# Kernel optimization log

Measured on AMD Instinct MI355X. Metric: run time of the kernel, lower is better.

## Reference

```python
import jax, jax.numpy as jnp
import numpy as np

B, H, W = 64, 512, 512
CD = 400                      # center_dims
MS_H = MS_W = 10              # max shifts
EPS = 1e-8
C_X = (H - CD) // 2           # 56
C_Y = (W - CD) // 2           # 56


def _conv_valid(x, k):
    # x: [B,h,w,1], k: [kh,kw,1,1] -> VALID conv, stride 1
    return jax.lax.conv_general_dilated(
        x, k, window_strides=(1, 1), padding='VALID',
        dimension_numbers=('NHWC', 'HWIO', 'NHWC'))


def setup_inputs() -> dict:
    key = jax.random.key(0)
    k1, k2 = jax.random.split(key)
    # smooth low-frequency template (so NCC peak neighborhood is positive -> log() finite)
    coarse = jax.random.normal(k1, (32, 32), dtype=jnp.float32)
    template = jax.image.resize(coarse, (H, W), method='bilinear')
    template = template - template.min() + 1.0  # keep positive-ish intensities
    noise = 0.05 * jax.random.normal(k2, (B, H, W, 1), dtype=jnp.float32)
    x = template[None, :, :, None] + noise
    return {'x': x, 'template': template}


def reference(x, template):
    # --- template normalization (init-time in the TF layer) ---
    tmpl = template[MS_W + C_X: H - (MS_W + C_X), MS_H + C_Y: W - (MS_H + C_Y)]  # [380,380]
    tmpl = tmpl[:, :, None, None].astype(jnp.float32)                            # HWIO
    t_zm = tmpl - jnp.mean(tmpl, axis=(0, 1), keepdims=True)
    t_var = jnp.sum(jnp.square(t_zm), axis=(0, 1), keepdims=True) + EPS          # [1,1,1,1]

    # --- image normalization ---
    Xc = x[:, C_X:H - C_X, C_Y:W - C_Y, :]                                       # [B,400,400,1]
    imgs_zm = Xc - jnp.mean(Xc, axis=(1, 2), keepdims=True)
    ones_k = jnp.ones_like(tmpl)
    localsum_sq = _conv_valid(jnp.square(Xc), ones_k)                            # [B,21,21,1]
    localsum = _conv_valid(Xc, ones_k)
    n_t = float(np.prod(tmpl.shape))
    imgs_var = localsum_sq - jnp.square(localsum) / n_t + EPS
    imgs_var = jnp.where(imgs_var < 0, jnp.zeros_like(imgs_var), imgs_var)

    # --- NCC ---
    denominator = jnp.sqrt(t_var * imgs_var)
    numerator = _conv_valid(imgs_zm, t_zm)
    ncc = numerator / denominator
    ncc = jnp.where(jnp.isnan(ncc), jnp.zeros_like(ncc), ncc)                    # [B,21,21,1]

    # --- integer argmax + gaussian (log-parabola) subpixel interpolation ---
    ncc2 = ncc[..., 0]                                                           # [B,21,21]
    ww = ncc2.shape[2]
    am = jnp.argmax(ncc2.reshape(B, -1), axis=1)
    sh_x = (am // ww).astype(jnp.int32)
    sh_y = (am % ww).astype(jnp.int32)
    log_ncc = jnp.log(ncc2)
    bidx = jnp.arange(B)

    def g(dx, dy):
        return log_ncc[bidx, sh_x + dx, sh_y + dy]

    log_xm1_y = g(-1, 0); log_xp1_y = g(1, 0)
    log_x_ym1 = g(0, -1); log_x_yp1 = g(0, 1)
    four_log_xy = 4.0 * g(0, 0)
    sh_x_n = (-(sh_x - MS_H)).astype(jnp.float32) - (log_xm1_y - log_xp1_y) / (
        2.0 * log_xm1_y - four_log_xy + 2.0 * log_xp1_y)
    sh_y_n = (-(sh_y - MS_W)).astype(jnp.float32) - (log_x_ym1 - log_x_yp1) / (
        2.0 * log_x_ym1 - four_log_xy + 2.0 * log_x_yp1)

    # --- bilinear translate: translations=[dx,dy]=[sh_y_n, sh_x_n]; out(r,c)=in(r-dy, c-dx), fill 0 ---
    def warp_one(img, dy, dx):
        rr = jnp.arange(H, dtype=jnp.float32)[:, None] - dy    # [H,1]
        cc = jnp.arange(W, dtype=jnp.float32)[None, :] - dx    # [1,W]
        r0 = jnp.floor(rr); c0 = jnp.floor(cc)
        wr = rr - r0; wc = cc - c0
        r0i = jnp.broadcast_to(r0.astype(jnp.int32), (H, W))
        c0i = jnp.broadcast_to(c0.astype(jnp.int32), (H, W))

        def samp(ri, ci):
            valid = (ri >= 0) & (ri < H) & (ci >= 0) & (ci < W)
            v = img[jnp.clip(ri, 0, H - 1), jnp.clip(ci, 0, W - 1)]
            return jnp.where(valid, v, 0.0)

        v00 = samp(r0i, c0i); v01 = samp(r0i, c0i + 1)
        v10 = samp(r0i + 1, c0i); v11 = samp(r0i + 1, c0i + 1)
        return (v00 * (1 - wr) * (1 - wc) + v01 * (1 - wr) * wc
                + v10 * wr * (1 - wc) + v11 * wr * wc)

    warped = jax.vmap(warp_one)(x[..., 0], sh_x_n, sh_y_n)     # [B,H,W]
    # transpose [0,2,1] then flatten, matching the TF layer's output layout
    return jnp.transpose(warped, (0, 2, 1)).reshape(B, H * W)
```

## Files before the change

### kernel.cpp

```cpp
#include <hip/hip_runtime.h>
#include <math.h>

#define HH 512
#define WW 512
#define NB 64
#define CXY 56
#define TOFF 66
#define TN 380
#define XN 400
#define NL 21
#define N_T 144400.0f
#define EPSF 1e-8f
#define NUT 32
#define SXS 424

#define TPART_S   0
#define TPART_S2  384
#define TSTATS    768
#define ROWSUM    1024
#define ROWSUMSQ  (ROWSUM + 537600)
#define CCPART2   1024
#define LOCALSUM  1076224
#define LOCALSQ   (LOCALSUM + 28224)
#define SHIFTS    1132672
#define SHIFTSI   (SHIFTS + 128)
#define EXACTN    (SHIFTSI + 128)
#define TSHIFT_F  (EXACTN + 384)
#define XF16      (TSHIFT_F + 1677312)

typedef _Float16 half2_t __attribute__((ext_vector_type(2)));
typedef _Float16 f16x8 __attribute__((ext_vector_type(8)));
typedef float f32x4 __attribute__((ext_vector_type(4)));

__global__ __launch_bounds__(128) void k_tstats1(const float* __restrict__ tpl,
                                                 float* __restrict__ ws) {
    int u = blockIdx.x;
    int l = threadIdx.x;
    const float* row = tpl + (TOFF + u) * WW + TOFF;
    float s = 0.f, s2 = 0.f;
    for (int v = l; v < TN; v += 128) { float t = row[v]; s += t; s2 += t * t; }
    for (int off = 32; off; off >>= 1) { s += __shfl_down(s, off); s2 += __shfl_down(s2, off); }
    __shared__ float rs[2], rs2[2];
    int wid = l >> 6;
    if ((l & 63) == 0) { rs[wid] = s; rs2[wid] = s2; }
    __syncthreads();
    if (l == 0) { ws[TPART_S + u] = rs[0] + rs[1]; ws[TPART_S2 + u] = rs2[0] + rs2[1]; }
}

__global__ __launch_bounds__(512) void k_tstats2(float* __restrict__ ws) {
    int l = threadIdx.x;
    float s  = (l < TN) ? ws[TPART_S + l]  : 0.f;
    float s2 = (l < TN) ? ws[TPART_S2 + l] : 0.f;
    for (int off = 32; off; off >>= 1) { s += __shfl_down(s, off); s2 += __shfl_down(s2, off); }
    __shared__ float rs[8], rs2[8];
    int wid = l >> 6;
    if ((l & 63) == 0) { rs[wid] = s; rs2[wid] = s2; }
    __syncthreads();
    if (l == 0) {
        float S = 0.f, S2 = 0.f;
        for (int k = 0; k < 8; ++k) { S += rs[k]; S2 += rs2[k]; }
        float mu = S / N_T;
        ws[TSTATS] = mu;
        ws[TSTATS + 1] = S2 - S * mu + EPSF;
    }
}

__global__ __launch_bounds__(256) void k_tshift(const float* __restrict__ tpl,
                                                float* __restrict__ ws) {
    int u = blockIdx.x;
    int j = blockIdx.y;
    float mu = ws[TSTATS];
    _Float16* dst = (_Float16*)(ws + TSHIFT_F) + ((size_t)j * 384 + u) * 416;
    for (int c = threadIdx.x; c < 416; c += 256) {
        float v = 0.f;
        int vs = c - j;
        if (u < TN && vs >= 0 && vs < TN) v = tpl[(TOFF + u) * WW + TOFF + vs] - mu;
        dst[c] = (_Float16)v;
    }
}

__global__ __launch_bounds__(256) void k_rowsum(const float* __restrict__ x,
                                                float* __restrict__ ws) {
    __shared__ float sm[4][416];
    int wid = threadIdx.x >> 6, lane = threadIdx.x & 63;
    int row = blockIdx.x * 4 + wid;
    int b = row / 416, p = row - b * 416;
    const float* xr = x + ((size_t)b * HH + (CXY + p)) * WW + CXY;
    _Float16* xh = (_Float16*)(ws + XF16) + ((size_t)b * 416 + p) * 416;
    float s = 0.f, s2 = 0.f;
    for (int v = lane; v < 416; v += 64) {
        float t = xr[v];
        sm[wid][v] = t;
        xh[v] = (_Float16)t;
        if (v < TN) { s += t; s2 += t * t; }
    }
    for (int off = 32; off; off >>= 1) { s += __shfl_down(s, off); s2 += __shfl_down(s2, off); }
    __syncthreads();
    if (lane == 0 && p < XN) {
        float* rs  = ws + ROWSUM   + (size_t)(b * XN + p) * NL;
        float* rq  = ws + ROWSUMSQ + (size_t)(b * XN + p) * NL;
        float w = s, w2 = s2;
        rs[0] = w; rq[0] = w2;
        for (int j = 1; j < NL; ++j) {
            float a = sm[wid][j - 1], bv = sm[wid][j + TN - 1];
            w  += bv - a;
            w2 += bv * bv - a * a;
            rs[j] = w; rq[j] = w2;
        }
    }
}

__global__ __launch_bounds__(512) void k_vert(float* __restrict__ ws) {
    int b = blockIdx.x, half = blockIdx.y, t = threadIdx.x;
    __shared__ float sm[XN * 22];
    const float* src = ws + (half ? ROWSUMSQ : ROWSUM) + (size_t)b * (XN * NL);
    for (int k = t; k < XN * NL; k += 512) {
        int p = k / NL, j = k - p * NL;
        sm[p * 22 + j] = src[k];
    }
    __syncthreads();
    if (t < NL * NL) {
        int i = t / NL, j = t - i * NL;
        const float* base = sm + i * 22 + j;
        float s0 = 0.f, s1 = 0.f, s2 = 0.f, s3 = 0.f;
        for (int p = 0; p < TN; p += 4) {
            s0 += base[p * 22];
            s1 += base[(p + 1) * 22];
            s2 += base[(p + 2) * 22];
            s3 += base[(p + 3) * 22];
        }
        ws[(half ? LOCALSQ : LOCALSUM) + b * (NL * NL) + t] = (s0 + s1) + (s2 + s3);
    }
}

__global__ __launch_bounds__(256) void k_ccm(float* __restrict__ ws) {
    const int bp = blockIdx.x, ut = blockIdx.y;
    const int U = 12 * ut;
    const int tid = threadIdx.x;
    const int lane = tid & 63, wv = tid >> 6;
    __shared__ __align__(16) _Float16 sX[2][32 * SXS];
    __shared__ float sD[4][16][34];

    {
        const _Float16* xh = (const _Float16*)(ws + XF16);
#pragma unroll
        for (int bb = 0; bb < 2; ++bb) {
            const _Float16* src0 = xh + ((size_t)(2 * bp + bb) * 416 + U) * 416;
            for (int c = tid; c < 32 * 52; c += 256) {
                int r = c / 52, c8 = c - r * 52;
                *reinterpret_cast<f16x8*>(&sX[bb][r * SXS + c8 * 8]) =
                    *reinterpret_cast<const f16x8*>(src0 + (size_t)r * 416 + c8 * 8);
            }
        }
    }
    __syncthreads();

    const _Float16* tsh = (const _Float16*)(ws + TSHIFT_F);
    const int r16 = lane & 15, h8 = (lane >> 4) * 8;
    const int rbase = (lane >> 4) * 4, cbase = lane & 15;
    const _Float16* bbA = &sX[0][r16 * SXS + h8];
    const _Float16* bbB = &sX[1][r16 * SXS + h8];

    for (int gi = 0; gi < 2; ++gi) {
        const int g = wv + 4 * gi;
        if (g >= 7) break;
        const int j0 = 3 * g;
        const _Float16* a0 = tsh + ((size_t)(j0    ) * 384 + U + r16) * 416 + h8;
        const _Float16* a1 = tsh + ((size_t)(j0 + 1) * 384 + U + r16) * 416 + h8;
        const _Float16* a2 = tsh + ((size_t)(j0 + 2) * 384 + U + r16) * 416 + h8;

        f32x4 z = {0.f, 0.f, 0.f, 0.f};
        f32x4 c000 = z, c001 = z, c010 = z, c011 = z, c020 = z, c021 = z;
        f32x4 c100 = z, c101 = z, c110 = z, c111 = z, c120 = z, c121 = z;
        f16x8 A0 = *reinterpret_cast<const f16x8*>(a0);
        f16x8 A1 = *reinterpret_cast<const f16x8*>(a1);
        f16x8 A2 = *reinterpret_cast<const f16x8*>(a2);
#pragma unroll
        for (int kc = 0; kc < 13; ++kc) {
            f16x8 N0 = A0, N1 = A1, N2 = A2;
            if (kc < 12) {
                N0 = *reinterpret_cast<const f16x8*>(a0 + (kc + 1) * 32);
                N1 = *reinterpret_cast<const f16x8*>(a1 + (kc + 1) * 32);
                N2 = *reinterpret_cast<const f16x8*>(a2 + (kc + 1) * 32);
            }
            f16x8 B00 = *reinterpret_cast<const f16x8*>(bbA + kc * 32);
            f16x8 B01 = *reinterpret_cast<const f16x8*>(bbA + 16 * SXS + kc * 32);
            f16x8 B10 = *reinterpret_cast<const f16x8*>(bbB + kc * 32);
            f16x8 B11 = *reinterpret_cast<const f16x8*>(bbB + 16 * SXS + kc * 32);
            __builtin_amdgcn_s_setprio(1);
            c000 = __builtin_amdgcn_mfma_f32_16x16x32_f16(A0, B00, c000, 0, 0, 0);
            c001 = __builtin_amdgcn_mfma_f32_16x16x32_f16(A0, B01, c001, 0, 0, 0);
            c100 = __builtin_amdgcn_mfma_f32_16x16x32_f16(A0, B10, c100, 0, 0, 0);
            c101 = __builtin_amdgcn_mfma_f32_16x16x32_f16(A0, B11, c101, 0, 0, 0);
            c010 = __builtin_amdgcn_mfma_f32_16x16x32_f16(A1, B00, c010, 0, 0, 0);
            c011 = __builtin_amdgcn_mfma_f32_16x16x32_f16(A1, B01, c011, 0, 0, 0);
            c110 = __builtin_amdgcn_mfma_f32_16x16x32_f16(A1, B10, c110, 0, 0, 0);
            c111 = __builtin_amdgcn_mfma_f32_16x16x32_f16(A1, B11, c111, 0, 0, 0);
            c020 = __builtin_amdgcn_mfma_f32_16x16x32_f16(A2, B00, c020, 0, 0, 0);
            c021 = __builtin_amdgcn_mfma_f32_16x16x32_f16(A2, B01, c021, 0, 0, 0);
            c120 = __builtin_amdgcn_mfma_f32_16x16x32_f16(A2, B10, c120, 0, 0, 0);
            c121 = __builtin_amdgcn_mfma_f32_16x16x32_f16(A2, B11, c121, 0, 0, 0);
            __builtin_amdgcn_s_setprio(0);
            A0 = N0; A1 = N1; A2 = N2;
        }

#pragma unroll
        for (int jj = 0; jj < 3; ++jj) {
#pragma unroll
            for (int bb = 0; bb < 2; ++bb) {
                f32x4 d0, d1;
                if (bb == 0) { d0 = (jj == 0) ? c000 : (jj == 1) ? c010 : c020;
                               d1 = (jj == 0) ? c001 : (jj == 1) ? c011 : c021; }
                else         { d0 = (jj == 0) ? c100 : (jj == 1) ? c110 : c120;
                               d1 = (jj == 0) ? c101 : (jj == 1) ? c111 : c121; }
#pragma unroll
                for (int q = 0; q < 4; ++q) {
                    sD[wv][rbase + q][cbase]      = d0[q];
                    sD[wv][rbase + q][16 + cbase] = d1[q];
                }
                if (lane < NL) {
                    float s = 0.f;
#pragma unroll
                    for (int row = 0; row < 12; ++row) s += sD[wv][row][row + lane];
                    ws[CCPART2 + ((size_t)((2 * bp + bb) * NUT + ut)) * 441
                       + lane * NL + (j0 + jj)] = s;
                }
            }
        }
    }
}

__global__ __launch_bounds__(512) void k_ncc(float* __restrict__ ws) {
    int b = blockIdx.x, t = threadIdx.x;
    __shared__ float vbuf[512];
    __shared__ int   ibuf[512];
    float val = -1e30f;
    if (t < NL * NL) {
        float num = 0.f;
        for (int ut = 0; ut < NUT; ++ut)
            num += ws[CCPART2 + ((size_t)(b * NUT + ut)) * 441 + t];
        float ls  = ws[LOCALSUM + b * (NL * NL) + t];
        float lsq = ws[LOCALSQ  + b * (NL * NL) + t];
        float ivar = lsq - ls * ls * (1.0f / N_T) + EPSF;
        if (ivar < 0.f) ivar = 0.f;
        float den = sqrtf(ws[TSTATS + 1] * ivar);
        float ncc = num / den;
        if (ncc != ncc) ncc = 0.f;
        val = ncc;
    }
    vbuf[t] = val; ibuf[t] = t;
    __syncthreads();
    for (int off = 256; off; off >>= 1) {
        if (t < off) {
            float v1 = vbuf[t], v2 = vbuf[t + off];
            int   i1 = ibuf[t], i2 = ibuf[t + off];
            if (v2 > v1 || (v2 == v1 && i2 < i1)) { vbuf[t] = v2; ibuf[t] = i2; }
        }
        __syncthreads();
    }
    if (t == 0) {
        int am = ibuf[0];
        ws[SHIFTSI + 2 * b]     = (float)(am / NL);
        ws[SHIFTSI + 2 * b + 1] = (float)(am % NL);
    }
}

__global__ __launch_bounds__(512) void k_exact1(const float* __restrict__ x,
                                                const float* __restrict__ tpl,
                                                float* __restrict__ ws) {
    const int b = blockIdx.x, k = blockIdx.y;
    const int sx = (int)ws[SHIFTSI + 2 * b];
    const int sy = (int)ws[SHIFTSI + 2 * b + 1];
    const int dxs[5] = {0, -1, 1, 0, 0};
    const int dys[5] = {0, 0, 0, -1, 1};
    const int px = min(max(sx + dxs[k], 0), NL - 1);
    const int py = min(max(sy + dys[k], 0), NL - 1);
    const float mu = ws[TSTATS];
    const int lane = threadIdx.x & 63, wv = threadIdx.x >> 6;
    float a = 0.f;
    for (int t = wv; t < TN; t += 8) {
        const float* trow = tpl + (TOFF + t) * WW + TOFF;
        const float* xrow = x + ((size_t)b * HH + (CXY + px + t)) * WW + CXY + py;
#pragma unroll
        for (int it = 0; it < 6; ++it) {
            int v = lane + it * 64;
            if (v < TN) a = fmaf(trow[v] - mu, xrow[v], a);
        }
    }
    for (int off = 32; off; off >>= 1) a += __shfl_down(a, off);
    __shared__ float part[8];
    if (lane == 0) part[wv] = a;
    __syncthreads();
    if (threadIdx.x == 0) {
        float s = 0.f;
        for (int w = 0; w < 8; ++w) s += part[w];
        ws[EXACTN + b * 5 + k] = s;
    }
}

__global__ __launch_bounds__(64) void k_sub(float* __restrict__ ws) {
    int b = threadIdx.x;
    if (b >= NB) return;
    int sx = (int)ws[SHIFTSI + 2 * b];
    int sy = (int)ws[SHIFTSI + 2 * b + 1];
    int lxm = max(sx - 1, 0), lxp = min(sx + 1, NL - 1);
    int lym = max(sy - 1, 0), lyp = min(sy + 1, NL - 1);
    float tvar = ws[TSTATS + 1];
    int cells[5] = { sx * NL + sy, lxm * NL + sy, lxp * NL + sy,
                     sx * NL + lym, sx * NL + lyp };
    float l[5];
    for (int k = 0; k < 5; ++k) {
        float num = ws[EXACTN + b * 5 + k];
        float ls  = ws[LOCALSUM + b * (NL * NL) + cells[k]];
        float lsq = ws[LOCALSQ  + b * (NL * NL) + cells[k]];
        float ivar = lsq - ls * ls * (1.0f / N_T) + EPSF;
        if (ivar < 0.f) ivar = 0.f;
        float ncc = num / sqrtf(tvar * ivar);
        if (ncc != ncc) ncc = 0.f;
        l[k] = logf(ncc);
    }
    float shx = -(float)(sx - 10) - (l[1] - l[2]) / (2.f * l[1] - 4.f * l[0] + 2.f * l[2]);
    float shy = -(float)(sy - 10) - (l[3] - l[4]) / (2.f * l[3] - 4.f * l[0] + 2.f * l[4]);
    ws[SHIFTS + 2 * b]     = shx;
    ws[SHIFTS + 2 * b + 1] = shy;
}

__global__ __launch_bounds__(256) void k_warp(const float* __restrict__ x,
                                              const float* __restrict__ ws,
                                              float* __restrict__ out) {
    const int b = blockIdx.z;
    const int R = blockIdx.x * 64;
    const int C = blockIdx.y * 64;
    const float dy = ws[SHIFTS + 2 * b], dx = ws[SHIFTS + 2 * b + 1];
    const int rlo = (int)floorf((float)R - dy);
    const int clo = (int)floorf((float)C - dx);
    const float wr = ((float)R - dy) - (float)rlo;
    const float wc = ((float)C - dx) - (float)clo;
    __shared__ float sm[66][67];
    const float* img = x + (size_t)b * (HH * WW);

    for (int k = threadIdx.x; k < 66 * 66; k += 256) {
        int kr = k / 66, kc = k - kr * 66;
        int ri = min(max(rlo + kr, 0), HH - 1);
        int ci = min(max(clo + kc, 0), WW - 1);
        sm[kr][kc] = img[ri * WW + ci];
    }
    __syncthreads();

    const int dr = threadIdx.x & 63;
    const int cq = threadIdx.x >> 6;
    const int r  = R + dr;
    const int r0 = rlo + dr;
    const float w00 = (1.f - wr) * (1.f - wc), w01 = (1.f - wr) * wc;
    const float w10 = wr * (1.f - wc),         w11 = wr * wc;
    const bool vr0 = (r0 >= 0) & (r0 < HH);
    const bool vr1 = (r0 + 1 >= 0) & (r0 + 1 < HH);
#pragma unroll
    for (int ci = 0; ci < 16; ++ci) {
        int dc = cq * 16 + ci;
        int c  = C + dc;
        int c0 = clo + dc;
        bool vc0 = (c0 >= 0) & (c0 < WW);
        bool vc1 = (c0 + 1 >= 0) & (c0 + 1 < WW);
        float v00 = (vr0 & vc0) ? sm[dr][dc]         : 0.f;
        float v01 = (vr0 & vc1) ? sm[dr][dc + 1]     : 0.f;
        float v10 = (vr1 & vc0) ? sm[dr + 1][dc]     : 0.f;
        float v11 = (vr1 & vc1) ? sm[dr + 1][dc + 1] : 0.f;
        float o = v00 * w00 + v01 * w01 + v10 * w10 + v11 * w11;
        out[(size_t)b * (HH * WW) + (size_t)c * HH + r] = o;
    }
}

extern "C" void kernel_launch(void* const* d_in, const int* in_sizes, int n_in,
                              void* d_out, int out_size, void* d_ws, size_t ws_size,
                              hipStream_t stream) {
    const float* x   = (const float*)d_in[0];
    const float* tpl = (const float*)d_in[1];
    float* out = (float*)d_out;
    float* ws  = (float*)d_ws;

    k_tstats1<<<TN, 128, 0, stream>>>(tpl, ws);
    k_tstats2<<<1, 512, 0, stream>>>(ws);
    k_tshift<<<dim3(384, NL), 256, 0, stream>>>(tpl, ws);
    k_rowsum<<<(NB * 416) / 4, 256, 0, stream>>>(x, ws);
    k_vert<<<dim3(NB, 2), 512, 0, stream>>>(ws);
    k_ccm<<<dim3(NB / 2, NUT), 256, 0, stream>>>(ws);
    k_ncc<<<NB, 512, 0, stream>>>(ws);
    k_exact1<<<dim3(NB, 5), 512, 0, stream>>>(x, tpl, ws);
    k_sub<<<1, 64, 0, stream>>>(ws);
    k_warp<<<dim3(8, 8, NB), dim3(256), 0, stream>>>(x, ws, out);
}
```

Baseline: 147.7 us.

## Fuse vertical box-sum into NCC kernel and widen cross-correlation blocks to 7 waves

After: 149.4 us. No clear change (+1.1%).

```diff
diff --git a/kernel.cpp b/kernel.cpp
--- a/kernel.cpp
+++ b/kernel.cpp
@@ -19,7 +19,6 @@
 #define TSTATS    768
 #define ROWSUM    1024
 #define ROWSUMSQ  (ROWSUM + 537600)
-#define CCPART2   1024
 #define LOCALSUM  1076224
 #define LOCALSQ   (LOCALSUM + 28224)
 #define SHIFTS    1132672
@@ -27,6 +26,7 @@
 #define EXACTN    (SHIFTSI + 128)
 #define TSHIFT_F  (EXACTN + 384)
 #define XF16      (TSHIFT_F + 1677312)
+#define CCPART2   8348416
 
 typedef _Float16 half2_t __attribute__((ext_vector_type(2)));
 typedef _Float16 f16x8 __attribute__((ext_vector_type(8)));
@@ -110,43 +110,20 @@
     }
 }
 
-__global__ __launch_bounds__(512) void k_vert(float* __restrict__ ws) {
-    int b = blockIdx.x, half = blockIdx.y, t = threadIdx.x;
-    __shared__ float sm[XN * 22];
-    const float* src = ws + (half ? ROWSUMSQ : ROWSUM) + (size_t)b * (XN * NL);
-    for (int k = t; k < XN * NL; k += 512) {
-        int p = k / NL, j = k - p * NL;
-        sm[p * 22 + j] = src[k];
-    }
-    __syncthreads();
-    if (t < NL * NL) {
-        int i = t / NL, j = t - i * NL;
-        const float* base = sm + i * 22 + j;
-        float s0 = 0.f, s1 = 0.f, s2 = 0.f, s3 = 0.f;
-        for (int p = 0; p < TN; p += 4) {
-            s0 += base[p * 22];
-            s1 += base[(p + 1) * 22];
-            s2 += base[(p + 2) * 22];
-            s3 += base[(p + 3) * 22];
-        }
-        ws[(half ? LOCALSQ : LOCALSUM) + b * (NL * NL) + t] = (s0 + s1) + (s2 + s3);
-    }
-}
-
-__global__ __launch_bounds__(256) void k_ccm(float* __restrict__ ws) {
+__global__ __launch_bounds__(512) void k_ccm(float* __restrict__ ws) {
     const int bp = blockIdx.x, ut = blockIdx.y;
     const int U = 12 * ut;
     const int tid = threadIdx.x;
     const int lane = tid & 63, wv = tid >> 6;
     __shared__ __align__(16) _Float16 sX[2][32 * SXS];
-    __shared__ float sD[4][16][34];
+    __shared__ float sD[7][16][34];
 
     {
         const _Float16* xh = (const _Float16*)(ws + XF16);
 #pragma unroll
         for (int bb = 0; bb < 2; ++bb) {
             const _Float16* src0 = xh + ((size_t)(2 * bp + bb) * 416 + U) * 416;
-            for (int c = tid; c < 32 * 52; c += 256) {
+            for (int c = tid; c < 32 * 52; c += 512) {
                 int r = c / 52, c8 = c - r * 52;
                 *reinterpret_cast<f16x8*>(&sX[bb][r * SXS + c8 * 8]) =
                     *reinterpret_cast<const f16x8*>(src0 + (size_t)r * 416 + c8 * 8);
@@ -155,16 +132,14 @@
     }
     __syncthreads();
 
-    const _Float16* tsh = (const _Float16*)(ws + TSHIFT_F);
-    const int r16 = lane & 15, h8 = (lane >> 4) * 8;
-    const int rbase = (lane >> 4) * 4, cbase = lane & 15;
-    const _Float16* bbA = &sX[0][r16 * SXS + h8];
-    const _Float16* bbB = &sX[1][r16 * SXS + h8];
-
-    for (int gi = 0; gi < 2; ++gi) {
-        const int g = wv + 4 * gi;
-        if (g >= 7) break;
-        const int j0 = 3 * g;
+    if (wv < 7) {
+        const _Float16* tsh = (const _Float16*)(ws + TSHIFT_F);
+        const int r16 = lane & 15, h8 = (lane >> 4) * 8;
+        const int rbase = (lane >> 4) * 4, cbase = lane & 15;
+        const _Float16* bbA = &sX[0][r16 * SXS + h8];
+        const _Float16* bbB = &sX[1][r16 * SXS + h8];
+
+        const int j0 = 3 * wv;
         const _Float16* a0 = tsh + ((size_t)(j0    ) * 384 + U + r16) * 416 + h8;
         const _Float16* a1 = tsh + ((size_t)(j0 + 1) * 384 + U + r16) * 416 + h8;
         const _Float16* a2 = tsh + ((size_t)(j0 + 2) * 384 + U + r16) * 416 + h8;
@@ -230,17 +205,53 @@
     }
 }
 
-__global__ __launch_bounds__(512) void k_ncc(float* __restrict__ ws) {
+__global__ __launch_bounds__(512) void k_vncc(float* __restrict__ ws) {
     int b = blockIdx.x, t = threadIdx.x;
+    __shared__ float big[XN * 22];
+    __shared__ float lsum[441];
     __shared__ float vbuf[512];
     __shared__ int   ibuf[512];
+
+    const float* srcS = ws + ROWSUM + (size_t)b * (XN * NL);
+    for (int k = t; k < XN * NL; k += 512) {
+        int p = k / NL, j = k - p * NL;
+        big[p * 22 + j] = srcS[k];
+    }
+    __syncthreads();
+    if (t < NL * NL) {
+        int i = t / NL, j = t - i * NL;
+        const float* base = big + i * 22 + j;
+        float s0 = 0.f, s1 = 0.f, s2 = 0.f, s3 = 0.f;
+        for (int p = 0; p < TN; p += 4) {
+            s0 += base[p * 22]; s1 += base[(p + 1) * 22];
+            s2 += base[(p + 2) * 22]; s3 += base[(p + 3) * 22];
+        }
+        float s = (s0 + s1) + (s2 + s3);
+        lsum[t] = s;
+        ws[LOCALSUM + b * (NL * NL) + t] = s;
+    }
+    __syncthreads();
+    const float* srcQ = ws + ROWSUMSQ + (size_t)b * (XN * NL);
+    for (int k = t; k < XN * NL; k += 512) {
+        int p = k / NL, j = k - p * NL;
+        big[p * 22 + j] = srcQ[k];
+    }
+    __syncthreads();
     float val = -1e30f;
     if (t < NL * NL) {
+        int i = t / NL, j = t - i * NL;
+        const float* base = big + i * 22 + j;
+        float s0 = 0.f, s1 = 0.f, s2 = 0.f, s3 = 0.f;
+        for (int p = 0; p < TN; p += 4) {
+            s0 += base[p * 22]; s1 += base[(p + 1) * 22];
+            s2 += base[(p + 2) * 22]; s3 += base[(p + 3) * 22];
+        }
+        float lsq = (s0 + s1) + (s2 + s3);
+        ws[LOCALSQ + b * (NL * NL) + t] = lsq;
         float num = 0.f;
         for (int ut = 0; ut < NUT; ++ut)
             num += ws[CCPART2 + ((size_t)(b * NUT + ut)) * 441 + t];
-        float ls  = ws[LOCALSUM + b * (NL * NL) + t];
-        float lsq = ws[LOCALSQ  + b * (NL * NL) + t];
+        float ls = lsum[t];
         float ivar = lsq - ls * ls * (1.0f / N_T) + EPSF;
         if (ivar < 0.f) ivar = 0.f;
         float den = sqrtf(ws[TSTATS + 1] * ivar);
@@ -383,9 +394,8 @@
     k_tstats2<<<1, 512, 0, stream>>>(ws);
     k_tshift<<<dim3(384, NL), 256, 0, stream>>>(tpl, ws);
     k_rowsum<<<(NB * 416) / 4, 256, 0, stream>>>(x, ws);
-    k_vert<<<dim3(NB, 2), 512, 0, stream>>>(ws);
-    k_ccm<<<dim3(NB / 2, NUT), 256, 0, stream>>>(ws);
-    k_ncc<<<NB, 512, 0, stream>>>(ws);
+    k_ccm<<<dim3(NB / 2, NUT), 512, 0, stream>>>(ws);
+    k_vncc<<<NB, 512, 0, stream>>>(ws);
     k_exact1<<<dim3(NB, 5), 512, 0, stream>>>(x, tpl, ws);
     k_sub<<<1, 64, 0, stream>>>(ws);
     k_warp<<<dim3(8, 8, NB), dim3(256), 0, stream>>>(x, ws, out);
```
